# Kernel optimization log

Hardware: AMD Instinct MI355X
Metric: run time of the kernel (lower is better)

The kernel has to match this reference:

```python
import jax, jax.numpy as jnp
import numpy as np
import math

D_MODEL = 1024
NUM_HEADS = 16
HEAD_DIM = D_MODEL // NUM_HEADS
BLOCK_SIZE = 64
THRESHOLD = 0.99


def setup_inputs() -> dict:
    key = jax.random.key(0)
    ks = jax.random.split(key, 12)
    B, S, D = 2, 2048, D_MODEL
    scale = 1.0 / math.sqrt(D)
    x = jax.random.normal(ks[0], (B, S, D), dtype=jnp.float32)
    G_ii = jax.random.uniform(ks[1], (B, S), dtype=jnp.float32)
    # Linear weights stored as [in, out]; applied as x @ W + b (matches nn.Linear math).
    Wq = jax.random.normal(ks[2], (D, D), dtype=jnp.float32) * scale
    bq = jnp.zeros((D,), dtype=jnp.float32)
    Wk = jax.random.normal(ks[3], (D, D), dtype=jnp.float32) * scale
    bk = jnp.zeros((D,), dtype=jnp.float32)
    Wv = jax.random.normal(ks[4], (D, D), dtype=jnp.float32) * scale
    bv = jnp.zeros((D,), dtype=jnp.float32)
    Wo = jax.random.normal(ks[5], (D, D), dtype=jnp.float32) * scale
    bo = jnp.zeros((D,), dtype=jnp.float32)
    return {"x": x, "G_ii": G_ii, "Wq": Wq, "bq": bq, "Wk": Wk, "bk": bk,
            "Wv": Wv, "bv": bv, "Wo": Wo, "bo": bo}


def reference(x, G_ii, Wq, bq, Wk, bk, Wv, bv, Wo, bo):
    B, S, D = x.shape
    H, hd, bs = NUM_HEADS, HEAD_DIM, BLOCK_SIZE
    nb = S // bs

    # Projections and head split: [B, H, S, hd]
    q = (x @ Wq + bq).reshape(B, S, H, hd).transpose(0, 2, 1, 3)
    k = (x @ Wk + bk).reshape(B, S, H, hd).transpose(0, 2, 1, 3)
    v = (x @ Wv + bv).reshape(B, S, H, hd).transpose(0, 2, 1, 3)

    # Per-query-block scattering energy keep mask: block kept iff max |G_ii| >= threshold
    energy = jnp.abs(G_ii)                              # [B, S]
    block_max = energy.reshape(B, nb, bs).max(axis=-1)  # [B, nb]
    keep = (block_max >= THRESHOLD)                     # [B, nb] bool
    row_keep = jnp.repeat(keep, bs, axis=1)             # [B, S]

    # Kept query blocks attend densely (non-causal) over all keys; skipped blocks output zero.
    scores = jnp.einsum('bhqd,bhkd->bhqk', q, k) / math.sqrt(hd)  # [B, H, S, S]
    attn = jax.nn.softmax(scores, axis=-1)
    out = jnp.einsum('bhqk,bhkd->bhqd', attn, v)                  # [B, H, S, hd]
    out = out * row_keep[:, None, :, None].astype(out.dtype)

    out = out.transpose(0, 2, 1, 3).reshape(B, S, D)
    return out @ Wo + bo
```

## Files before the change

kernel.cpp:

```cpp
#include <hip/hip_runtime.h>
#include <math.h>

#define D_MODEL   1024
#define NUM_HEADS 16
#define HEAD_DIM  64
#define BS        64
#define NB        32
#define S_LEN     2048
#define BATCH     2
#define M_ROWS    (BATCH * S_LEN)
#define THRESH    0.99f
#define SCEXP     0.18033688f
#define SPLITK    4
#define NSLOT     66
#define SLOTB     (NSLOT * 16)

typedef __attribute__((ext_vector_type(8))) short bf16x8;
typedef __attribute__((ext_vector_type(8))) _Float16 f16x8;
typedef __attribute__((ext_vector_type(2))) __fp16 fp16v2;
typedef __attribute__((ext_vector_type(4))) float f32x4;

__device__ __forceinline__ unsigned short f2bf(float f) {
    unsigned int u = __float_as_uint(f);
    u += 0x7fff + ((u >> 16) & 1);
    return (unsigned short)(u >> 16);
}

__device__ __forceinline__ unsigned int pkrtz(float a, float b) {
    fp16v2 r = __builtin_amdgcn_cvt_pkrtz(a, b);
    return __builtin_bit_cast(unsigned int, r);
}

__device__ __forceinline__ void gload16(const void* gptr, void* lptr) {
    __builtin_amdgcn_global_load_lds(
        (const __attribute__((address_space(1))) void*)gptr,
        (__attribute__((address_space(3))) void*)lptr, 16, 0, 0);
}

__global__ __launch_bounds__(256) void prep_kernel(
    const float* __restrict__ x, const float* __restrict__ G,
    const float* __restrict__ Wq, const float* __restrict__ Wk,
    const float* __restrict__ Wv, const float* __restrict__ Wo,
    unsigned short* __restrict__ xb, unsigned short* __restrict__ wcat,
    unsigned short* __restrict__ wot, int* __restrict__ keep, int* __restrict__ work)
{
    const int bid = blockIdx.x, tid = threadIdx.x;
    __shared__ float T[64][65];

    if (bid < 2048) {
        size_t i = ((size_t)bid * 256 + tid) * 8;
        float4 a = *(const float4*)(x + i);
        float4 b = *(const float4*)(x + i + 4);
        uint4 o;
        o.x = (unsigned int)f2bf(a.x) | ((unsigned int)f2bf(a.y) << 16);
        o.y = (unsigned int)f2bf(a.z) | ((unsigned int)f2bf(a.w) << 16);
        o.z = (unsigned int)f2bf(b.x) | ((unsigned int)f2bf(b.y) << 16);
        o.w = (unsigned int)f2bf(b.z) | ((unsigned int)f2bf(b.w) << 16);
        *(uint4*)(xb + i) = o;
    } else if (bid < 3072) {
        int i = bid - 2048;
        int mat = i >> 8, rem = i & 255;
        int k0 = (rem & 15) * 64, n0 = (rem >> 4) * 64;
        const float* W = (mat == 0) ? Wq : (mat == 1) ? Wk : (mat == 2) ? Wv : Wo;
        int rr = tid >> 4, c4 = (tid & 15) * 4;
        #pragma unroll
        for (int j = 0; j < 4; j++) {
            int row = rr + j * 16;
            float4 v = *(const float4*)(W + (size_t)(k0 + row) * 1024 + n0 + c4);
            T[row][c4 + 0] = v.x; T[row][c4 + 1] = v.y;
            T[row][c4 + 2] = v.z; T[row][c4 + 3] = v.w;
        }
        __syncthreads();
        unsigned short* dst = (mat < 3) ? (wcat + (size_t)mat * 1024 * 1024) : wot;
        #pragma unroll
        for (int j = 0; j < 4; j++) {
            int n = rr + j * 16;
            unsigned int lo = (unsigned int)f2bf(T[c4 + 0][n]) | ((unsigned int)f2bf(T[c4 + 1][n]) << 16);
            unsigned int hi = (unsigned int)f2bf(T[c4 + 2][n]) | ((unsigned int)f2bf(T[c4 + 3][n]) << 16);
            *(uint2*)(dst + (size_t)(n0 + n) * 1024 + k0 + c4) = make_uint2(lo, hi);
        }
    } else {
        if (tid < 64) {
            int t = tid;
            const float4* g = (const float4*)(G + (size_t)t * 64);
            float mx = 0.f;
            #pragma unroll
            for (int j = 0; j < 16; j++) {
                float4 v = g[j];
                mx = fmaxf(mx, fmaxf(fmaxf(fabsf(v.x), fabsf(v.y)), fmaxf(fabsf(v.z), fabsf(v.w))));
            }
            bool k = (mx >= THRESH);
            unsigned long long bal = __ballot(k);
            unsigned int mk0 = (unsigned int)bal, mk1 = (unsigned int)(bal >> 32);
            int nk0 = __popc(mk0), nk1 = __popc(mk1);
            int ND0 = (nk0 + 1) >> 1, ND1 = (nk1 + 1) >> 1;
            keep[t] = k ? 1 : 0;
            int tb = t & 31, bb = t >> 5;
            unsigned int mb = bb ? mk1 : mk0;
            unsigned int msk = (tb == 0) ? 0u : ((1u << tb) - 1u);
            int rank = __popc(mb & msk);
            int rd   = __popc(~mb & msk);
            int base = bb ? 2 * ND0 : 0;
            int dbase = 2 * ND0 + 2 * ND1;
            int doff = bb ? (32 - nk0) : 0;
            if (k)  work[1 + base + rank] = t;
            else    work[1 + dbase + doff + rd] = t | (1 << 8);
            if (t == 0) {
                work[0] = ND0 + ND1;
                if (nk0 & 1) work[1 + nk0] = (31 - __clz(mk0)) | (2 << 8);
                if (nk1 & 1) work[1 + 2 * ND0 + nk1] = (63 - __clz(mk1)) | (2 << 8);
                int total = dbase + (64 - nk0 - nk1);
                for (int j = total; j < NSLOT; j++) work[1 + j] = (2 << 8);
            }
        }
    }
}

__global__ __launch_bounds__(256, 3) void gemm_qkv(
    const unsigned short* __restrict__ A, const unsigned short* __restrict__ Bt,
    const float* __restrict__ bq, const float* __restrict__ bk, const float* __restrict__ bv,
    const int* __restrict__ keep, unsigned short* __restrict__ qk, unsigned short* __restrict__ vt)
{
    const int n0 = blockIdx.x * 128, m0 = blockIdx.y * 128;
    const int tid = threadIdx.x, w = tid >> 6, lane = tid & 63;
    const int quad = lane >> 4, l16 = lane & 15;
    const int wm = w >> 1, wn = w & 1;
    const int kindb = n0 >> 10;
    if (kindb == 0 && !(keep[2 * blockIdx.y] | keep[2 * blockIdx.y + 1])) return;

    __shared__ union {
        struct { unsigned short As[2][128 * 32]; unsigned short Bs[2][128 * 32]; } s;
        unsigned short qkr[128 * 136];
        unsigned short vr[128 * 136];
    } u;

    f32x4 acc[4][4];
    #pragma unroll
    for (int mt = 0; mt < 4; mt++)
        #pragma unroll
        for (int nt = 0; nt < 4; nt++) acc[mt][nt] = (f32x4){0.f, 0.f, 0.f, 0.f};

    #define QSTAGE(it_, p_)                                                             \
        {                                                                               \
            int k0_ = (it_) * 32;                                                       \
            _Pragma("unroll")                                                           \
            for (int j = 0; j < 2; j++) {                                               \
                int s_ = w * 128 + j * 64 + lane; int row = s_ >> 2, cl = s_ & 3;       \
                int c = cl ^ ((row >> 1) & 3);                                          \
                gload16(A + (size_t)(m0 + row) * 1024 + k0_ + c * 8,                    \
                        &u.s.As[p_][(w * 128 + j * 64) * 8]);                           \
            }                                                                           \
            _Pragma("unroll")                                                           \
            for (int j = 0; j < 2; j++) {                                               \
                int s_ = w * 128 + j * 64 + lane; int row = s_ >> 2, cl = s_ & 3;       \
                int c = cl ^ ((row >> 1) & 3);                                          \
                gload16(Bt + (size_t)(n0 + row) * 1024 + k0_ + c * 8,                   \
                        &u.s.Bs[p_][(w * 128 + j * 64) * 8]);                           \
            }                                                                           \
        }

    QSTAGE(0, 0)

    for (int it = 0; it < 32; it++) {
        const int p = it & 1;
        __syncthreads();
        if (it + 1 < 32) QSTAGE(it + 1, (it + 1) & 1)

        bf16x8 af[4], bfr[4];
        #pragma unroll
        for (int mt = 0; mt < 4; mt++) {
            int row = wm * 64 + mt * 16 + l16;
            int cl = quad ^ ((row >> 1) & 3);
            af[mt] = *(const bf16x8*)&u.s.As[p][(row * 4 + cl) * 8];
        }
        #pragma unroll
        for (int nt = 0; nt < 4; nt++) {
            int row = wn * 64 + nt * 16 + l16;
            int cl = quad ^ ((row >> 1) & 3);
            bfr[nt] = *(const bf16x8*)&u.s.Bs[p][(row * 4 + cl) * 8];
        }
        #pragma unroll
        for (int mt = 0; mt < 4; mt++)
            #pragma unroll
            for (int nt = 0; nt < 4; nt++)
                acc[mt][nt] = __builtin_amdgcn_mfma_f32_16x16x32_bf16(af[mt], bfr[nt], acc[mt][nt], 0, 0, 0);
    }
    __syncthreads();

    if (kindb < 2) {
        const float* bp = (kindb == 0) ? bq : bk;
        const float sc = (kindb == 0) ? SCEXP : 1.0f;
        #pragma unroll
        for (int nt = 0; nt < 4; nt++) {
            int coll = wn * 64 + nt * 16 + l16;
            float bb = bp[(n0 & 1023) + coll];
            #pragma unroll
            for (int mt = 0; mt < 4; mt++)
                #pragma unroll
                for (int r = 0; r < 4; r++) {
                    int row = wm * 64 + mt * 16 + quad * 4 + r;
                    u.qkr[row * 136 + coll] = f2bf((acc[mt][nt][r] + bb) * sc);
                }
        }
        __syncthreads();
        #pragma unroll
        for (int i = 0; i < 8; i++) {
            int s_ = tid + i * 256;
            int row = s_ >> 4, c16 = s_ & 15;
            uint4 v = *(const uint4*)&u.qkr[row * 136 + c16 * 8];
            *(uint4*)(qk + (size_t)(m0 + row) * 2048 + n0 + c16 * 8) = v;
        }
    } else {
        #pragma unroll
        for (int nt = 0; nt < 4; nt++) {
            int coll = wn * 64 + nt * 16 + l16;
            float bb = bv[(n0 - 2048) + coll];
            #pragma unroll
            for (int mt = 0; mt < 4; mt++) {
                int s0 = wm * 64 + mt * 16 + quad * 4;
                uint2 pv;
                pv.x = pkrtz(acc[mt][nt][0] + bb, acc[mt][nt][1] + bb);
                pv.y = pkrtz(acc[mt][nt][2] + bb, acc[mt][nt][3] + bb);
                *(uint2*)&u.vr[coll * 136 + s0] = pv;
            }
        }
        __syncthreads();
        const int b_ = m0 >> 11, sbase = m0 & 2047;
        #pragma unroll
        for (int i = 0; i < 8; i++) {
            int s_ = tid + i * 256;
            int coll = s_ >> 4, ch = s_ & 15;
            uint4 v = *(const uint4*)&u.vr[coll * 136 + ch * 8];
            int colg = n0 - 2048 + coll;
            int h_ = colg >> 6, d = colg & 63;
            *(uint4*)(vt + ((size_t)(b_ * NUM_HEADS + h_) * HEAD_DIM + d) * 2048 + sbase + ch * 8) = v;
        }
    }
}

__global__ __launch_bounds__(256, 4) void gemm_out(
    const unsigned short* __restrict__ A, const unsigned short* __restrict__ Bt,
    const float* __restrict__ bo, const int* __restrict__ keep, float* __restrict__ out)
{
    const int n0 = blockIdx.x * 128, m0 = blockIdx.y * 64;
    const int tid = threadIdx.x, w = tid >> 6, lane = tid & 63;
    const int quad = lane >> 4, l16 = lane & 15;
    const int wm = w >> 1, wn = w & 1;

    if (!keep[blockIdx.y]) {
        #pragma unroll
        for (int i = 0; i < 8; i++) {
            int s_ = tid + i * 256;
            int row = s_ >> 5, c = (s_ & 31) * 4;
            *(float4*)(out + (size_t)(m0 + row) * 1024 + n0 + c) = *(const float4*)(bo + n0 + c);
        }
        return;
    }

    __shared__ unsigned short Asl[2][64 * 32];
    __shared__ unsigned short Bsl[2][128 * 32];

    f32x4 acc[2][4];
    #pragma unroll
    for (int mt = 0; mt < 2; mt++)
        #pragma unroll
        for (int nt = 0; nt < 4; nt++) acc[mt][nt] = (f32x4){0.f, 0.f, 0.f, 0.f};

    #define OSTAGE(it_, p_)                                                             \
        {                                                                               \
            int k0_ = (it_) * 32;                                                       \
            { int s_ = w * 64 + lane; int row = s_ >> 2, cl = s_ & 3;                   \
              int c = cl ^ ((row >> 1) & 3);                                            \
              gload16(A + (size_t)(m0 + row) * 1024 + k0_ + c * 8,                      \
                      &Asl[p_][(w * 64) * 8]); }                                        \
            _Pragma("unroll")                                                           \
            for (int j = 0; j < 2; j++) {                                               \
                int s_ = w * 128 + j * 64 + lane; int row = s_ >> 2, cl = s_ & 3;       \
                int c = cl ^ ((row >> 1) & 3);                                          \
                gload16(Bt + (size_t)(n0 + row) * 1024 + k0_ + c * 8,                   \
                        &Bsl[p_][(w * 128 + j * 64) * 8]);                              \
            }                                                                           \
        }

    OSTAGE(0, 0)

    for (int it = 0; it < 32; it++) {
        const int p = it & 1;
        __syncthreads();
        if (it + 1 < 32) OSTAGE(it + 1, (it + 1) & 1)

        bf16x8 af[2], bfr[4];
        #pragma unroll
        for (int mt = 0; mt < 2; mt++) {
            int row = wm * 32 + mt * 16 + l16;
            int cl = quad ^ ((row >> 1) & 3);
            af[mt] = *(const bf16x8*)&Asl[p][(row * 4 + cl) * 8];
        }
        #pragma unroll
        for (int nt = 0; nt < 4; nt++) {
            int row = wn * 64 + nt * 16 + l16;
            int cl = quad ^ ((row >> 1) & 3);
            bfr[nt] = *(const bf16x8*)&Bsl[p][(row * 4 + cl) * 8];
        }
        #pragma unroll
        for (int mt = 0; mt < 2; mt++)
            #pragma unroll
            for (int nt = 0; nt < 4; nt++)
                acc[mt][nt] = __builtin_amdgcn_mfma_f32_16x16x32_bf16(af[mt], bfr[nt], acc[mt][nt], 0, 0, 0);
    }

    #pragma unroll
    for (int nt = 0; nt < 4; nt++) {
        int col = n0 + wn * 64 + nt * 16 + l16;
        float bb = bo[col];
        #pragma unroll
        for (int mt = 0; mt < 2; mt++) {
            int mb = m0 + wm * 32 + mt * 16 + quad * 4;
            #pragma unroll
            for (int r = 0; r < 4; r++)
                out[(size_t)(mb + r) * 1024 + col] = acc[mt][nt][r] + bb;
        }
    }
}

__global__ __launch_bounds__(256, 3) void attn_kernel(
    const unsigned short* __restrict__ qk, const unsigned short* __restrict__ Vtg,
    const int* __restrict__ work,
    unsigned short* __restrict__ opart, float* __restrict__ lpart)
{
    const int bx = blockIdx.x, half = blockIdx.y;
    const int dpair = bx >> 4, h = bx & 15;
    const int tid  = threadIdx.x;
    const int w    = tid >> 6, lane = tid & 63;
    const int quad = lane >> 4, l16 = lane & 15;

    if (dpair >= work[0]) return;
    const int j0 = 2 * dpair, j1 = j0 + 1;
    const int t0 = work[1 + j0] & 63, t1 = work[1 + j1] & 63;
    const int b = t0 >> 5, qb0 = t0 & 31, qb1 = t1 & 31;

    __shared__ unsigned short Kbuf[2][BS * HEAD_DIM];
    __shared__ unsigned short Vbuf[2][HEAD_DIM * BS];
    __shared__ unsigned short Pt[4][2][16 * 64];

    const int KEYS = S_LEN / SPLITK;
    const int NCH  = KEYS / BS;
    const unsigned short* Qb = qk + (size_t)(b * S_LEN) * 2048 + h * 64;
    const unsigned short* Kb = qk + (size_t)(b * S_LEN + half * KEYS) * 2048 + 1024 + h * 64;
    const unsigned short* Vb = Vtg + (size_t)(b * NUM_HEADS + h) * HEAD_DIM * 2048 + half * KEYS;

    const int qrow0 = qb0 * BS + w * 16 + l16;
    const int qrow1 = qb1 * BS + w * 16 + l16;
    bf16x8 qf0[2], qf1[2];
    #pragma unroll
    for (int ks = 0; ks < 2; ks++) {
        qf0[ks] = *(const bf16x8*)(Qb + (size_t)qrow0 * 2048 + ks * 32 + quad * 8);
        qf1[ks] = *(const bf16x8*)(Qb + (size_t)qrow1 * 2048 + ks * 32 + quad * 8);
    }

    f32x4 o0[4], o1[4];
    #pragma unroll
    for (int mt = 0; mt < 4; mt++) { o0[mt] = (f32x4){0.f,0.f,0.f,0.f}; o1[mt] = (f32x4){0.f,0.f,0.f,0.f}; }
    float l0 = 0.f, l1 = 0.f;

    const int sA = w * 128 + lane, sB = sA + 64;
    const int rA = sA >> 3, cA = (sA & 7) ^ (rA & 7);
    const int rB = sB >> 3, cB = (sB & 7) ^ (rB & 7);
    const size_t koA = (size_t)rA * 2048 + cA * 8, koB = (size_t)rB * 2048 + cB * 8;

    uint4 kr0, kr1, vr0, vr1;
    #define LOADREGS(kc_)                                                       \
        {                                                                       \
            const unsigned short* kg_ = Kb + (size_t)(kc_) * BS * 2048;         \
            const unsigned short* vg_ = Vb + (size_t)(kc_) * BS;                \
            kr0 = *(const uint4*)(kg_ + koA); kr1 = *(const uint4*)(kg_ + koB); \
            vr0 = *(const uint4*)(vg_ + koA); vr1 = *(const uint4*)(vg_ + koB); \
        }
    #define WRITELDS(pb_)                                                       \
        {                                                                       \
            *(uint4*)&Kbuf[pb_][(size_t)sA * 8] = kr0;                          \
            *(uint4*)&Kbuf[pb_][(size_t)sB * 8] = kr1;                          \
            *(uint4*)&Vbuf[pb_][(size_t)sA * 8] = vr0;                          \
            *(uint4*)&Vbuf[pb_][(size_t)sB * 8] = vr1;                          \
        }

    LOADREGS(0)
    WRITELDS(0)
    __syncthreads();

    #pragma unroll
    for (int kc = 0; kc < NCH; kc++) {
        const int p = kc & 1;
        if (kc + 1 < NCH) LOADREGS(kc + 1)

        f32x4 st0[4], st1[4];
        __builtin_amdgcn_s_setprio(1);
        #pragma unroll
        for (int mt = 0; mt < 4; mt++) {
            f32x4 a0 = {0.f,0.f,0.f,0.f}, a1 = {0.f,0.f,0.f,0.f};
            #pragma unroll
            for (int ks = 0; ks < 2; ks++) {
                int kk = mt * 16 + l16;
                bf16x8 kf = *(const bf16x8*)&Kbuf[p][(size_t)(kk * 8 + ((ks * 4 + quad) ^ (kk & 7))) * 8];
                a0 = __builtin_amdgcn_mfma_f32_16x16x32_bf16(kf, qf0[ks], a0, 0, 0, 0);
                a1 = __builtin_amdgcn_mfma_f32_16x16x32_bf16(kf, qf1[ks], a1, 0, 0, 0);
            }
            st0[mt] = a0; st1[mt] = a1;
        }
        __builtin_amdgcn_s_setprio(0);

        float sum0 = 0.f, sum1 = 0.f;
        #pragma unroll
        for (int mt = 0; mt < 4; mt++) {
            int c16 = 2 * mt + (quad >> 1);
            int off = (c16 ^ (l16 & 7)) * 8 + (quad & 1) * 4;
            float e00 = __builtin_amdgcn_exp2f(st0[mt][0]);
            float e01 = __builtin_amdgcn_exp2f(st0[mt][1]);
            float e02 = __builtin_amdgcn_exp2f(st0[mt][2]);
            float e03 = __builtin_amdgcn_exp2f(st0[mt][3]);
            sum0 += (e00 + e01) + (e02 + e03);
            *(uint2*)&Pt[w][0][l16 * 64 + off] = make_uint2(pkrtz(e00, e01), pkrtz(e02, e03));
            float e10 = __builtin_amdgcn_exp2f(st1[mt][0]);
            float e11 = __builtin_amdgcn_exp2f(st1[mt][1]);
            float e12 = __builtin_amdgcn_exp2f(st1[mt][2]);
            float e13 = __builtin_amdgcn_exp2f(st1[mt][3]);
            sum1 += (e10 + e11) + (e12 + e13);
            *(uint2*)&Pt[w][1][l16 * 64 + off] = make_uint2(pkrtz(e10, e11), pkrtz(e12, e13));
        }
        sum0 += __shfl_xor(sum0, 16, 64);
        sum0 += __shfl_xor(sum0, 32, 64);
        sum1 += __shfl_xor(sum1, 16, 64);
        sum1 += __shfl_xor(sum1, 32, 64);
        l0 += sum0; l1 += sum1;

        __builtin_amdgcn_s_setprio(1);
        #pragma unroll
        for (int ks = 0; ks < 2; ks++) {
            int poff = ((4 * ks + quad) ^ (l16 & 7)) * 8;
            f16x8 pf0 = *(const f16x8*)&Pt[w][0][l16 * 64 + poff];
            f16x8 pf1 = *(const f16x8*)&Pt[w][1][l16 * 64 + poff];
            #pragma unroll
            for (int mt = 0; mt < 4; mt++) {
                int d = mt * 16 + l16;
                f16x8 vf = *(const f16x8*)&Vbuf[p][(size_t)(d * 8 + ((ks * 4 + quad) ^ (d & 7))) * 8];
                o0[mt] = __builtin_amdgcn_mfma_f32_16x16x32_f16(vf, pf0, o0[mt], 0, 0, 0);
                o1[mt] = __builtin_amdgcn_mfma_f32_16x16x32_f16(vf, pf1, o1[mt], 0, 0, 0);
            }
        }
        __builtin_amdgcn_s_setprio(0);

        if (kc + 1 < NCH) {
            WRITELDS(p ^ 1)
            __syncthreads();
        }
    }

    {
        unsigned short* ob = opart + ((size_t)(half * SLOTB + j0 * 16 + h)) * 4096 + tid * 16;
        uint4 w0, w1;
        w0.x = pkrtz(o0[0][0], o0[0][1]); w0.y = pkrtz(o0[0][2], o0[0][3]);
        w0.z = pkrtz(o0[1][0], o0[1][1]); w0.w = pkrtz(o0[1][2], o0[1][3]);
        w1.x = pkrtz(o0[2][0], o0[2][1]); w1.y = pkrtz(o0[2][2], o0[2][3]);
        w1.z = pkrtz(o0[3][0], o0[3][1]); w1.w = pkrtz(o0[3][2], o0[3][3]);
        *(uint4*)ob = w0;
        *(uint4*)(ob + 8) = w1;
    }
    {
        unsigned short* ob = opart + ((size_t)(half * SLOTB + j1 * 16 + h)) * 4096 + tid * 16;
        uint4 w0, w1;
        w0.x = pkrtz(o1[0][0], o1[0][1]); w0.y = pkrtz(o1[0][2], o1[0][3]);
        w0.z = pkrtz(o1[1][0], o1[1][1]); w0.w = pkrtz(o1[1][2], o1[1][3]);
        w1.x = pkrtz(o1[2][0], o1[2][1]); w1.y = pkrtz(o1[2][2], o1[2][3]);
        w1.z = pkrtz(o1[3][0], o1[3][1]); w1.w = pkrtz(o1[3][2], o1[3][3]);
        *(uint4*)ob = w0;
        *(uint4*)(ob + 8) = w1;
    }
    if (quad == 0) {
        lpart[((size_t)half * SLOTB + j0 * 16 + h) * 64 + w * 16 + l16] = l0;
        lpart[((size_t)half * SLOTB + j1 * 16 + h) * 64 + w * 16 + l16] = l1;
    }
}

__global__ __launch_bounds__(256) void attn_combine(
    const unsigned short* __restrict__ opart, const float* __restrict__ lpart,
    const int* __restrict__ work, unsigned short* __restrict__ attn_out)
{
    const int bx = blockIdx.x;
    const int pair = bx >> 4, h = bx & 15;
    const int tid  = threadIdx.x;
    const int w    = tid >> 6, lane = tid & 63;
    const int quad = lane >> 4, l16 = lane & 15;

    const int e = work[1 + pair];
    const int flag = e >> 8, t = e & 63;
    if (flag == 2) return;
    const int b = t >> 5, qblk = t & 31;
    unsigned short* ablk = attn_out + ((size_t)(b * S_LEN + qblk * BS)) * D_MODEL + h * HEAD_DIM;

    if (flag == 1) {
        uint4 z = make_uint4(0, 0, 0, 0);
        #pragma unroll
        for (int i = 0; i < 2; i++) {
            int u = tid + i * 256;
            int row = u >> 3, c8 = (u & 7) * 8;
            *(uint4*)(ablk + (size_t)row * D_MODEL + c8) = z;
        }
        return;
    }

    __shared__ float Obuf[4][HEAD_DIM * 17];

    float osum[16];
    #pragma unroll
    for (int j = 0; j < 16; j++) osum[j] = 0.f;
    float lsum = 0.f;
    #pragma unroll
    for (int hf = 0; hf < SPLITK; hf++) {
        const f16x8* pp = (const f16x8*)(opart + ((size_t)hf * SLOTB + bx) * 4096 + tid * 16);
        f16x8 a0 = pp[0], a1 = pp[1];
        #pragma unroll
        for (int j = 0; j < 8; j++) {
            osum[j]     += (float)a0[j];
            osum[8 + j] += (float)a1[j];
        }
        lsum += lpart[((size_t)hf * SLOTB + bx) * 64 + w * 16 + l16];
    }
    float inv = 1.0f / lsum;

    #pragma unroll
    for (int mt = 0; mt < 4; mt++)
        #pragma unroll
        for (int r = 0; r < 4; r++)
            Obuf[w][(mt * 16 + quad * 4 + r) * 17 + l16] = osum[mt * 4 + r] * inv;
    #pragma unroll
    for (int i = 0; i < 4; i++) {
        int uu = lane + 64 * i;
        int row = uu >> 4, d4 = (uu & 15) * 4;
        float x0 = Obuf[w][(d4 + 0) * 17 + row];
        float x1 = Obuf[w][(d4 + 1) * 17 + row];
        float x2 = Obuf[w][(d4 + 2) * 17 + row];
        float x3 = Obuf[w][(d4 + 3) * 17 + row];
        unsigned int lo = (unsigned int)f2bf(x0) | ((unsigned int)f2bf(x1) << 16);
        unsigned int hi = (unsigned int)f2bf(x2) | ((unsigned int)f2bf(x3) << 16);
        *(uint2*)(ablk + (size_t)(w * 16 + row) * D_MODEL + d4) = make_uint2(lo, hi);
    }
}

extern "C" void kernel_launch(void* const* d_in, const int* in_sizes, int n_in,
                              void* d_out, int out_size, void* d_ws, size_t ws_size,
                              hipStream_t stream) {
    const float* x  = (const float*)d_in[0];
    const float* G  = (const float*)d_in[1];
    const float* Wq = (const float*)d_in[2];
    const float* bq = (const float*)d_in[3];
    const float* Wk = (const float*)d_in[4];
    const float* bk = (const float*)d_in[5];
    const float* Wv = (const float*)d_in[6];
    const float* bv = (const float*)d_in[7];
    const float* Wo = (const float*)d_in[8];
    const float* bo = (const float*)d_in[9];
    float* out = (float*)d_out;

    char* wsp = (char*)d_ws;
    int* keep = (int*)wsp;
    int* work = keep + 64;
    unsigned short* xb    = (unsigned short*)(wsp + 1024);
    unsigned short* wcat  = xb + (size_t)M_ROWS * D_MODEL;
    unsigned short* wot   = wcat + (size_t)3 * 1024 * 1024;
    unsigned short* qk    = wot + (size_t)1024 * 1024;
    unsigned short* vt    = qk + (size_t)M_ROWS * 2048;
    unsigned short* attnb = vt + (size_t)BATCH * NUM_HEADS * HEAD_DIM * 2048;
    unsigned short* opart = attnb + (size_t)M_ROWS * D_MODEL;
    float* lpart = (float*)(opart + (size_t)SPLITK * SLOTB * 4096);

    prep_kernel<<<3073, 256, 0, stream>>>(x, G, Wq, Wk, Wv, Wo, xb, wcat, wot, keep, work);

    gemm_qkv<<<dim3(3072 / 128, M_ROWS / 128), 256, 0, stream>>>(
        xb, wcat, bq, bk, bv, keep, qk, vt);

    attn_kernel<<<dim3(32 * 16, SPLITK), 256, 0, stream>>>(qk, vt, work, opart, lpart);
    attn_combine<<<SLOTB, 256, 0, stream>>>(opart, lpart, work, attnb);

    gemm_out<<<dim3(1024 / 128, M_ROWS / 64), 256, 0, stream>>>(attnb, wot, bo, keep, out);
}
```

Baseline: 176.7 us.

## Process four query blocks per attention workgroup to reuse K/V tiles

Each attention workgroup now handles four kept query blocks instead of two, so every K/V chunk loaded into shared memory feeds twice as many MFMAs. The work list is padded to multiples of four per batch (with duplicated dummy entries), NSLOT grows accordingly, and the grid halves. It trades higher register and LDS use, with launch bounds relaxed to two waves per SIMD, plus possible wasted padding work and fewer blocks for load balance.

```diff
diff --git a/kernel.cpp b/kernel.cpp
--- a/kernel.cpp
+++ b/kernel.cpp
@@ -12,7 +12,7 @@
 #define THRESH    0.99f
 #define SCEXP     0.18033688f
 #define SPLITK    4
-#define NSLOT     66
+#define NSLOT     70
 #define SLOTB     (NSLOT * 16)
 
 typedef __attribute__((ext_vector_type(8))) short bf16x8;
@@ -93,22 +93,24 @@
             unsigned long long bal = __ballot(k);
             unsigned int mk0 = (unsigned int)bal, mk1 = (unsigned int)(bal >> 32);
             int nk0 = __popc(mk0), nk1 = __popc(mk1);
-            int ND0 = (nk0 + 1) >> 1, ND1 = (nk1 + 1) >> 1;
+            int ND0 = (nk0 + 3) >> 2, ND1 = (nk1 + 3) >> 2;
             keep[t] = k ? 1 : 0;
             int tb = t & 31, bb = t >> 5;
             unsigned int mb = bb ? mk1 : mk0;
             unsigned int msk = (tb == 0) ? 0u : ((1u << tb) - 1u);
             int rank = __popc(mb & msk);
             int rd   = __popc(~mb & msk);
-            int base = bb ? 2 * ND0 : 0;
-            int dbase = 2 * ND0 + 2 * ND1;
+            int base = bb ? 4 * ND0 : 0;
+            int dbase = 4 * ND0 + 4 * ND1;
             int doff = bb ? (32 - nk0) : 0;
             if (k)  work[1 + base + rank] = t;
             else    work[1 + dbase + doff + rd] = t | (1 << 8);
             if (t == 0) {
                 work[0] = ND0 + ND1;
-                if (nk0 & 1) work[1 + nk0] = (31 - __clz(mk0)) | (2 << 8);
-                if (nk1 & 1) work[1 + 2 * ND0 + nk1] = (63 - __clz(mk1)) | (2 << 8);
+                int last0 = (nk0 > 0) ? (31 - __clz(mk0)) : 0;
+                for (int j = nk0; j < 4 * ND0; j++) work[1 + j] = last0 | (2 << 8);
+                int last1 = (nk1 > 0) ? (63 - __clz(mk1)) : 0;
+                for (int j = nk1; j < 4 * ND1; j++) work[1 + 4 * ND0 + j] = last1 | (2 << 8);
                 int total = dbase + (64 - nk0 - nk1);
                 for (int j = total; j < NSLOT; j++) work[1 + j] = (2 << 8);
             }
@@ -323,25 +325,26 @@
     }
 }
 
-__global__ __launch_bounds__(256, 3) void attn_kernel(
+__global__ __launch_bounds__(256, 2) void attn_kernel(
     const unsigned short* __restrict__ qk, const unsigned short* __restrict__ Vtg,
     const int* __restrict__ work,
     unsigned short* __restrict__ opart, float* __restrict__ lpart)
 {
     const int bx = blockIdx.x, half = blockIdx.y;
-    const int dpair = bx >> 4, h = bx & 15;
+    const int dquad = bx >> 4, h = bx & 15;
     const int tid  = threadIdx.x;
     const int w    = tid >> 6, lane = tid & 63;
     const int quad = lane >> 4, l16 = lane & 15;
 
-    if (dpair >= work[0]) return;
-    const int j0 = 2 * dpair, j1 = j0 + 1;
-    const int t0 = work[1 + j0] & 63, t1 = work[1 + j1] & 63;
-    const int b = t0 >> 5, qb0 = t0 & 31, qb1 = t1 & 31;
+    if (dquad >= work[0]) return;
+    const int j0 = 4 * dquad;
+    const int qb[4] = { work[1 + j0 + 0] & 31, work[1 + j0 + 1] & 31,
+                        work[1 + j0 + 2] & 31, work[1 + j0 + 3] & 31 };
+    const int b = (work[1 + j0] & 63) >> 5;
 
     __shared__ unsigned short Kbuf[2][BS * HEAD_DIM];
     __shared__ unsigned short Vbuf[2][HEAD_DIM * BS];
-    __shared__ unsigned short Pt[4][2][16 * 64];
+    __shared__ unsigned short Pt[4][4][16 * 64];
 
     const int KEYS = S_LEN / SPLITK;
     const int NCH  = KEYS / BS;
@@ -349,19 +352,21 @@
     const unsigned short* Kb = qk + (size_t)(b * S_LEN + half * KEYS) * 2048 + 1024 + h * 64;
     const unsigned short* Vb = Vtg + (size_t)(b * NUM_HEADS + h) * HEAD_DIM * 2048 + half * KEYS;
 
-    const int qrow0 = qb0 * BS + w * 16 + l16;
-    const int qrow1 = qb1 * BS + w * 16 + l16;
-    bf16x8 qf0[2], qf1[2];
-    #pragma unroll
-    for (int ks = 0; ks < 2; ks++) {
-        qf0[ks] = *(const bf16x8*)(Qb + (size_t)qrow0 * 2048 + ks * 32 + quad * 8);
-        qf1[ks] = *(const bf16x8*)(Qb + (size_t)qrow1 * 2048 + ks * 32 + quad * 8);
-    }
-
-    f32x4 o0[4], o1[4];
-    #pragma unroll
-    for (int mt = 0; mt < 4; mt++) { o0[mt] = (f32x4){0.f,0.f,0.f,0.f}; o1[mt] = (f32x4){0.f,0.f,0.f,0.f}; }
-    float l0 = 0.f, l1 = 0.f;
+    bf16x8 qf[4][2];
+    #pragma unroll
+    for (int q = 0; q < 4; q++) {
+        int qrow = qb[q] * BS + w * 16 + l16;
+        #pragma unroll
+        for (int ks = 0; ks < 2; ks++)
+            qf[q][ks] = *(const bf16x8*)(Qb + (size_t)qrow * 2048 + ks * 32 + quad * 8);
+    }
+
+    f32x4 o[4][4];
+    #pragma unroll
+    for (int q = 0; q < 4; q++)
+        #pragma unroll
+        for (int mt = 0; mt < 4; mt++) o[q][mt] = (f32x4){0.f, 0.f, 0.f, 0.f};
+    float l[4] = {0.f, 0.f, 0.f, 0.f};
 
     const int sA = w * 128 + lane, sB = sA + 64;
     const int rA = sA >> 3, cA = (sA & 7) ^ (rA & 7);
@@ -393,58 +398,63 @@
         const int p = kc & 1;
         if (kc + 1 < NCH) LOADREGS(kc + 1)
 
-        f32x4 st0[4], st1[4];
-        __builtin_amdgcn_s_setprio(1);
-        #pragma unroll
-        for (int mt = 0; mt < 4; mt++) {
-            f32x4 a0 = {0.f,0.f,0.f,0.f}, a1 = {0.f,0.f,0.f,0.f};
-            #pragma unroll
-            for (int ks = 0; ks < 2; ks++) {
-                int kk = mt * 16 + l16;
-                bf16x8 kf = *(const bf16x8*)&Kbuf[p][(size_t)(kk * 8 + ((ks * 4 + quad) ^ (kk & 7))) * 8];
-                a0 = __builtin_amdgcn_mfma_f32_16x16x32_bf16(kf, qf0[ks], a0, 0, 0, 0);
-                a1 = __builtin_amdgcn_mfma_f32_16x16x32_bf16(kf, qf1[ks], a1, 0, 0, 0);
+        #pragma unroll
+        for (int qp = 0; qp < 2; qp++) {
+            f32x4 st0[4], st1[4];
+            __builtin_amdgcn_s_setprio(1);
+            #pragma unroll
+            for (int mt = 0; mt < 4; mt++) {
+                f32x4 a0 = {0.f,0.f,0.f,0.f}, a1 = {0.f,0.f,0.f,0.f};
+                #pragma unroll
+                for (int ks = 0; ks < 2; ks++) {
+                    int kk = mt * 16 + l16;
+                    bf16x8 kf = *(const bf16x8*)&Kbuf[p][(size_t)(kk * 8 + ((ks * 4 + quad) ^ (kk & 7))) * 8];
+                    a0 = __builtin_amdgcn_mfma_f32_16x16x32_bf16(kf, qf[2 * qp][ks], a0, 0, 0, 0);
+                    a1 = __builtin_amdgcn_mfma_f32_16x16x32_bf16(kf, qf[2 * qp + 1][ks], a1, 0, 0, 0);
+                }
+                st0[mt] = a0; st1[mt] = a1;
             }
-            st0[mt] = a0; st1[mt] = a1;
-        }
-        __builtin_amdgcn_s_setprio(0);
-
-        float sum0 = 0.f, sum1 = 0.f;
-        #pragma unroll
-        for (int mt = 0; mt < 4; mt++) {
-            int c16 = 2 * mt + (quad >> 1);
-            int off = (c16 ^ (l16 & 7)) * 8 + (quad & 1) * 4;
-            float e00 = __builtin_amdgcn_exp2f(st0[mt][0]);
-            float e01 = __builtin_amdgcn_exp2f(st0[mt][1]);
-            float e02 = __builtin_amdgcn_exp2f(st0[mt][2]);
-            float e03 = __builtin_amdgcn_exp2f(st0[mt][3]);
-            sum0 += (e00 + e01) + (e02 + e03);
-            *(uint2*)&Pt[w][0][l16 * 64 + off] = make_uint2(pkrtz(e00, e01), pkrtz(e02, e03));
-            float e10 = __builtin_amdgcn_exp2f(st1[mt][0]);
-            float e11 = __builtin_amdgcn_exp2f(st1[mt][1]);
-            float e12 = __builtin_amdgcn_exp2f(st1[mt][2]);
-            float e13 = __builtin_amdgcn_exp2f(st1[mt][3]);
-            sum1 += (e10 + e11) + (e12 + e13);
-            *(uint2*)&Pt[w][1][l16 * 64 + off] = make_uint2(pkrtz(e10, e11), pkrtz(e12, e13));
-        }
-        sum0 += __shfl_xor(sum0, 16, 64);
-        sum0 += __shfl_xor(sum0, 32, 64);
-        sum1 += __shfl_xor(sum1, 16, 64);
-        sum1 += __shfl_xor(sum1, 32, 64);
-        l0 += sum0; l1 += sum1;
+            __builtin_amdgcn_s_setprio(0);
+
+            float sum0 = 0.f, sum1 = 0.f;
+            #pragma unroll
+            for (int mt = 0; mt < 4; mt++) {
+                int c16 = 2 * mt + (quad >> 1);
+                int off = (c16 ^ (l16 & 7)) * 8 + (quad & 1) * 4;
+                float e00 = __builtin_amdgcn_exp2f(st0[mt][0]);
+                float e01 = __builtin_amdgcn_exp2f(st0[mt][1]);
+                float e02 = __builtin_amdgcn_exp2f(st0[mt][2]);
+                float e03 = __builtin_amdgcn_exp2f(st0[mt][3]);
+                sum0 += (e00 + e01) + (e02 + e03);
+                *(uint2*)&Pt[w][2 * qp][l16 * 64 + off] = make_uint2(pkrtz(e00, e01), pkrtz(e02, e03));
+                float e10 = __builtin_amdgcn_exp2f(st1[mt][0]);
+                float e11 = __builtin_amdgcn_exp2f(st1[mt][1]);
+                float e12 = __builtin_amdgcn_exp2f(st1[mt][2]);
+                float e13 = __builtin_amdgcn_exp2f(st1[mt][3]);
+                sum1 += (e10 + e11) + (e12 + e13);
+                *(uint2*)&Pt[w][2 * qp + 1][l16 * 64 + off] = make_uint2(pkrtz(e10, e11), pkrtz(e12, e13));
+            }
+            sum0 += __shfl_xor(sum0, 16, 64);
+            sum0 += __shfl_xor(sum0, 32, 64);
+            sum1 += __shfl_xor(sum1, 16, 64);
+            sum1 += __shfl_xor(sum1, 32, 64);
+            l[2 * qp] += sum0; l[2 * qp + 1] += sum1;
+        }
 
         __builtin_amdgcn_s_setprio(1);
         #pragma unroll
         for (int ks = 0; ks < 2; ks++) {
             int poff = ((4 * ks + quad) ^ (l16 & 7)) * 8;
-            f16x8 pf0 = *(const f16x8*)&Pt[w][0][l16 * 64 + poff];
-            f16x8 pf1 = *(const f16x8*)&Pt[w][1][l16 * 64 + poff];
+            f16x8 pf[4];
+            #pragma unroll
+            for (int q = 0; q < 4; q++) pf[q] = *(const f16x8*)&Pt[w][q][l16 * 64 + poff];
             #pragma unroll
             for (int mt = 0; mt < 4; mt++) {
                 int d = mt * 16 + l16;
                 f16x8 vf = *(const f16x8*)&Vbuf[p][(size_t)(d * 8 + ((ks * 4 + quad) ^ (d & 7))) * 8];
-                o0[mt] = __builtin_amdgcn_mfma_f32_16x16x32_f16(vf, pf0, o0[mt], 0, 0, 0);
-                o1[mt] = __builtin_amdgcn_mfma_f32_16x16x32_f16(vf, pf1, o1[mt], 0, 0, 0);
+                #pragma unroll
+                for (int q = 0; q < 4; q++)
+                    o[q][mt] = __builtin_amdgcn_mfma_f32_16x16x32_f16(vf, pf[q], o[q][mt], 0, 0, 0);
             }
         }
         __builtin_amdgcn_s_setprio(0);
@@ -455,29 +465,17 @@
         }
     }
 
-    {
-        unsigned short* ob = opart + ((size_t)(half * SLOTB + j0 * 16 + h)) * 4096 + tid * 16;
+    #pragma unroll
+    for (int q = 0; q < 4; q++) {
+        unsigned short* ob = opart + ((size_t)(half * SLOTB + (j0 + q) * 16 + h)) * 4096 + tid * 16;
         uint4 w0, w1;
-        w0.x = pkrtz(o0[0][0], o0[0][1]); w0.y = pkrtz(o0[0][2], o0[0][3]);
-        w0.z = pkrtz(o0[1][0], o0[1][1]); w0.w = pkrtz(o0[1][2], o0[1][3]);
-        w1.x = pkrtz(o0[2][0], o0[2][1]); w1.y = pkrtz(o0[2][2], o0[2][3]);
-        w1.z = pkrtz(o0[3][0], o0[3][1]); w1.w = pkrtz(o0[3][2], o0[3][3]);
+        w0.x = pkrtz(o[q][0][0], o[q][0][1]); w0.y = pkrtz(o[q][0][2], o[q][0][3]);
+        w0.z = pkrtz(o[q][1][0], o[q][1][1]); w0.w = pkrtz(o[q][1][2], o[q][1][3]);
+        w1.x = pkrtz(o[q][2][0], o[q][2][1]); w1.y = pkrtz(o[q][2][2], o[q][2][3]);
+        w1.z = pkrtz(o[q][3][0], o[q][3][1]); w1.w = pkrtz(o[q][3][2], o[q][3][3]);
         *(uint4*)ob = w0;
         *(uint4*)(ob + 8) = w1;
-    }
-    {
-        unsigned short* ob = opart + ((size_t)(half * SLOTB + j1 * 16 + h)) * 4096 + tid * 16;
-        uint4 w0, w1;
-        w0.x = pkrtz(o1[0][0], o1[0][1]); w0.y = pkrtz(o1[0][2], o1[0][3]);
-        w0.z = pkrtz(o1[1][0], o1[1][1]); w0.w = pkrtz(o1[1][2], o1[1][3]);
-        w1.x = pkrtz(o1[2][0], o1[2][1]); w1.y = pkrtz(o1[2][2], o1[2][3]);
-        w1.z = pkrtz(o1[3][0], o1[3][1]); w1.w = pkrtz(o1[3][2], o1[3][3]);
-        *(uint4*)ob = w0;
-        *(uint4*)(ob + 8) = w1;
-    }
-    if (quad == 0) {
-        lpart[((size_t)half * SLOTB + j0 * 16 + h) * 64 + w * 16 + l16] = l0;
-        lpart[((size_t)half * SLOTB + j1 * 16 + h) * 64 + w * 16 + l16] = l1;
+        if (quad == 0) lpart[((size_t)half * SLOTB + (j0 + q) * 16 + h) * 64 + w * 16 + l16] = l[q];
     }
 }
 
@@ -578,7 +576,7 @@
     gemm_qkv<<<dim3(3072 / 128, M_ROWS / 128), 256, 0, stream>>>(
         xb, wcat, bq, bk, bv, keep, qk, vt);
 
-    attn_kernel<<<dim3(32 * 16, SPLITK), 256, 0, stream>>>(qk, vt, work, opart, lpart);
+    attn_kernel<<<dim3(16 * 16, SPLITK), 256, 0, stream>>>(qk, vt, work, opart, lpart);
     attn_combine<<<SLOTB, 256, 0, stream>>>(opart, lpart, work, attnb);
 
     gemm_out<<<dim3(1024 / 128, M_ROWS / 64), 256, 0, stream>>>(attnb, wot, bo, keep, out);
```

After: 217.8 us. 23.3% more time.
